# Kernel optimization log

Measured on AMD Instinct MI355X. Metric: run time of the kernel, lower is better.

Reference implementation:

```python
import jax, jax.numpy as jnp
import numpy as np

WALK_LENGTH = 8
NUM_WALKS = 5
BIRTH_DEATH_EPS = 0.1
TOLERANCE = 0.1
HALF_WIN = 16          # window is [cur-16, cur+17)
TEMP = 5.0
NEG = -1e9
EPS = 1e-8


def setup_inputs() -> dict:
    key = jax.random.key(0)
    k1, k2 = jax.random.split(key)
    seq_len, hidden = 8192, 1024
    hidden_states = jax.random.normal(k1, (seq_len, hidden), dtype=jnp.float32)
    violation_indices = jax.random.randint(k2, (1024,), 0, seq_len)
    return {"hidden_states": hidden_states, "violation_indices": violation_indices}


def _cycle_ok(row_sq, i, j, k):
    # TriadicReciprocityCheck.check_cycle, simplified algebraically:
    # M_ab = outer(b,a)/|a|^2 etc., so P = M_ca M_bc M_ab
    #      = outer(a,a) * |b|^2 |c|^2 / ((|a|^2+eps)(|b|^2+eps)(|c|^2+eps))
    # => trace(P) == fro_norm(P) == |a|^2|b|^2|c|^2 / denom  (outer(a,a) has trace=fro=|a|^2)
    na, nb, nc = row_sq[i], row_sq[j], row_sq[k]
    tr = na * nb * nc / ((na + EPS) * (nb + EPS) * (nc + EPS))
    dev = jnp.abs(tr - jnp.round(tr))
    return (dev <= TOLERANCE) & (tr <= 1.5)


def _walk(key, start, states_norm, row_sq, violation_indices):
    seq_len = states_norm.shape[0]
    offsets = jnp.arange(-HALF_WIN, HALF_WIN + 1)  # 33 local positions

    def step(carry, _):
        key, cur, prev, plen, min_sim, done, detected, aborts, restarts = carry
        key, k_samp, k_restart = jax.random.split(key, 3)
        idxs = cur + offsets
        valid = (idxs >= 0) & (idxs < seq_len)
        g = states_norm[jnp.clip(idxs, 0, seq_len - 1)]      # [33, D]
        sims = g @ states_norm[cur]                           # [33]
        logits = jnp.where(valid & (idxs != cur), sims, NEG) * TEMP
        # up to 3 multinomial attempts, each gated by the triadic reciprocity check
        samp_keys = jax.random.split(k_samp, 3)
        picks = jax.vmap(lambda k: jax.random.categorical(k, logits))(samp_keys)
        cands = cur + offsets[picks]                          # [3] candidate nodes
        ok = jax.vmap(lambda c: (plen < 2) | _cycle_ok(row_sq, prev, cur, c))(cands)
        found = jnp.any(ok)
        first = jnp.argmax(ok)
        n_aborts = jnp.where(found, first, 3).astype(jnp.int32)  # failed attempts
        cand = cands[first]
        # 'jump mental tracks': teleport to a random violation node if all attempts fail
        r = jax.random.randint(k_restart, (), 0, violation_indices.shape[0])
        restart_node = violation_indices[r]
        sim = states_norm[cur] @ states_norm[cand]
        new_min = jnp.minimum(min_sim, sim)  # path_sims min (NOT reset on restart)
        closed = found & (cand == start) & (plen > 2)
        act = ~done
        aborts = aborts + jnp.where(act, n_aborts, 0).astype(jnp.int32)
        restarts = restarts + jnp.where(act & ~found, 1, 0).astype(jnp.int32)
        detected = detected | (act & closed & (new_min < BIRTH_DEATH_EPS))
        done = done | (act & closed)
        cur2 = jnp.where(found, cand, restart_node)
        prev2 = jnp.where(found, cur, restart_node)
        plen2 = jnp.where(found, plen + 1, 1).astype(jnp.int32)
        ms2 = jnp.where(found, new_min, min_sim)
        cur = jnp.where(act, cur2, cur)
        prev = jnp.where(act, prev2, prev)
        plen = jnp.where(act, plen2, plen)
        min_sim = jnp.where(act, ms2, min_sim)
        return (key, cur, prev, plen, min_sim, done, detected, aborts, restarts), None

    init = (key, start, start, jnp.int32(1), jnp.float32(1e9),
            jnp.bool_(False), jnp.bool_(False), jnp.int32(0), jnp.int32(0))
    carry, _ = jax.lax.scan(step, init, None, length=WALK_LENGTH)
    return carry[6], carry[7], carry[8]  # detected, aborts, restarts


def reference(hidden_states, violation_indices):
    states_norm = hidden_states / (jnp.linalg.norm(hidden_states, axis=1, keepdims=True) + EPS)
    row_sq = jnp.sum(hidden_states * hidden_states, axis=1)  # |h_i|^2, for cycle check
    nv = violation_indices.shape[0]
    keys = jax.random.split(jax.random.key(42), nv * NUM_WALKS).reshape(nv, NUM_WALKS)
    walk = lambda k, s: _walk(k, s, states_norm, row_sq, violation_indices)
    det, ab, rs = jax.vmap(lambda ks, s: jax.vmap(lambda k: walk(k, s))(ks))(keys, violation_indices)
    instability_detected = jnp.any(det, axis=1)  # [num_violations] bool
    return instability_detected, jnp.sum(ab), jnp.sum(rs)
```

## Files before the change

kernel.cpp:

```cpp
#include <hip/hip_runtime.h>
#include <stdint.h>
#include <math.h>


#define HID        1024
#define NUM_WALKS  5
#define WALK_LEN   8
#define HALF_WIN   16
#define E_THRESH   1.6487212707001282

#define CENTERS    16
#define SROWS      32

__device__ __forceinline__ void tf2x32(uint32_t k0, uint32_t k1,
                                       uint32_t& x0, uint32_t& x1) {
  uint32_t ks2 = k0 ^ k1 ^ 0x1BD11BDAu;
  x0 += k0; x1 += k1;
#define TFR(r) { x0 += x1; x1 = (x1 << (r)) | (x1 >> (32 - (r))); x1 ^= x0; }
  TFR(13) TFR(15) TFR(26) TFR(6)
  x0 += k1;  x1 += ks2 + 1u;
  TFR(17) TFR(29) TFR(16) TFR(24)
  x0 += ks2; x1 += k0 + 2u;
  TFR(13) TFR(15) TFR(26) TFR(6)
  x0 += k0;  x1 += k1 + 3u;
  TFR(17) TFR(29) TFR(16) TFR(24)
  x0 += k1;  x1 += ks2 + 4u;
  TFR(13) TFR(15) TFR(26) TFR(6)
  x0 += ks2; x1 += k0 + 5u;
#undef TFR
}

__device__ __forceinline__ uint32_t tf_fold(uint32_t k0, uint32_t k1,
                                            uint32_t c0, uint32_t c1) {
  tf2x32(k0, k1, c0, c1);
  return c0 ^ c1;
}

__device__ __forceinline__ double fast_neg_log(uint32_t bits) {
  const uint32_t k = bits >> 9;
  if (k == 0) return 87.33654475055310899;
  const float u  = (float)k * 1.1920928955078125e-7f;
  const float l2 = __log2f(u);
  return (double)l2 * -0.6931471805599453;
}

__global__ __launch_bounds__(512) void band_fused_kernel(
    const float* __restrict__ H, double* __restrict__ sumsq,
    double* __restrict__ E, int* __restrict__ out, int out_n, int seq_len) {
  __shared__ __align__(16) float  tile[SROWS][HID];
  __shared__ double ssq[SROWS];

  if (blockIdx.x == 0) {
    for (int t = threadIdx.x; t < out_n; t += 512) out[t] = 0;
  }

  int wg = blockIdx.x;
  {
    const int nwg = gridDim.x;
    if ((nwg & 7) == 0) wg = (wg & 7) * (nwg >> 3) + (wg >> 3);
  }
  const int wid  = (int)(threadIdx.x >> 6);
  const int lane = (int)(threadIdx.x & 63);
  const int i0   = wg * CENTERS;
  const float4* __restrict__ H4 = (const float4*)H;

#pragma unroll
  for (int rr = 0; rr < 4; ++rr) {
    const int local = wid * 4 + rr;
    const int row   = i0 + local;
    if (row < seq_len) {
      const float4* src = H4 + ((size_t)row << 8);
      float4* dst = (float4*)&tile[local][0];
      double acc = 0.0;
#pragma unroll
      for (int k = 0; k < 4; ++k) {
        float4 x = src[lane + (k << 6)];
        dst[lane + (k << 6)] = x;
        acc += (double)x.x * x.x + (double)x.y * x.y
             + (double)x.z * x.z + (double)x.w * x.w;
      }
#pragma unroll
      for (int off = 32; off; off >>= 1) acc += __shfl_xor(acc, off);
      if (lane == 0) {
        ssq[local] = acc;
        if (local < CENTERS) sumsq[row] = acc;
      }
    }
  }
  __syncthreads();

#pragma unroll
  for (int cc = 0; cc < 2; ++cc) {
    const int cl = wid * 2 + cc;
    const int i  = i0 + cl;
    if (i >= seq_len) continue;

    float a[16];
    {
      const float4* rc = (const float4*)&tile[cl][0];
#pragma unroll
      for (int k = 0; k < 4; ++k) {
        float4 x = rc[lane + (k << 6)];
        a[4*k+0] = x.x; a[4*k+1] = x.y; a[4*k+2] = x.z; a[4*k+3] = x.w;
      }
    }
    const double ni = sqrt(ssq[cl]) + 1e-8;

    double p[16];
#pragma unroll
    for (int d = 1; d <= 16; ++d) {
      const float4* rb = (const float4*)&tile[cl + d][0];
      float ps = 0.0f;
#pragma unroll
      for (int k = 0; k < 4; ++k) {
        float4 x = rb[lane + (k << 6)];
        ps += a[4*k+0] * x.x + a[4*k+1] * x.y
            + a[4*k+2] * x.z + a[4*k+3] * x.w;
      }
      p[d-1] = (double)ps;
    }

#pragma unroll
    for (int v = 0; v < 8; ++v) {
      double send = (lane & 32) ? p[v] : p[v+8];
      double recv = __shfl_xor(send, 32);
      double mine = (lane & 32) ? p[v+8] : p[v];
      p[v] = mine + recv;
    }
#pragma unroll
    for (int v = 0; v < 4; ++v) {
      double send = (lane & 16) ? p[v] : p[v+4];
      double recv = __shfl_xor(send, 16);
      double mine = (lane & 16) ? p[v+4] : p[v];
      p[v] = mine + recv;
    }
#pragma unroll
    for (int v = 0; v < 2; ++v) {
      double send = (lane & 8) ? p[v] : p[v+2];
      double recv = __shfl_xor(send, 8);
      double mine = (lane & 8) ? p[v+2] : p[v];
      p[v] = mine + recv;
    }
    {
      double send = (lane & 4) ? p[0] : p[1];
      double recv = __shfl_xor(send, 4);
      double mine = (lane & 4) ? p[1] : p[0];
      p[0] = mine + recv;
    }
    p[0] += __shfl_xor(p[0], 2);
    p[0] += __shfl_xor(p[0], 1);

    const int v = ((lane >> 2) & 1) | (((lane >> 3) & 1) << 1)
                | (((lane >> 4) & 1) << 2) | (((lane >> 5) & 1) << 3);
    const int d = v + 1;
    if ((lane & 3) == 0 && i + d < seq_len) {
      const double s  = p[0] / (ni * (sqrt(ssq[cl + d]) + 1e-8));
      const double Ev = exp(5.0 * s);
      E[(size_t)i * 33 + 16 + d]       = Ev;
      E[(size_t)(i + d) * 33 + 16 - d] = Ev;
    }
  }
}

__global__ __launch_bounds__(256) void rowsq_kernel(
    const float* __restrict__ H, double* __restrict__ sumsq,
    int* __restrict__ out, int out_n, int seq_len) {
  if (blockIdx.x == 0) {
    for (int t = threadIdx.x; t < out_n; t += 256) out[t] = 0;
  }
  const int row  = (int)((blockIdx.x * blockDim.x + threadIdx.x) >> 6);
  const int lane = threadIdx.x & 63;
  if (row >= seq_len) return;
  const float4* r = (const float4*)(H + (size_t)row * HID);
  double acc = 0.0;
#pragma unroll
  for (int k = 0; k < 4; ++k) {
    float4 x = r[lane + (k << 6)];
    acc += (double)x.x * x.x + (double)x.y * x.y
         + (double)x.z * x.z + (double)x.w * x.w;
  }
#pragma unroll
  for (int off = 32; off; off >>= 1) acc += __shfl_xor(acc, off);
  if (lane == 0) sumsq[row] = acc;
}

__global__ __launch_bounds__(256) void walk_pre_kernel(
    const double* __restrict__ E, const double* __restrict__ sumsq,
    const int* __restrict__ viol, int* __restrict__ out,
    int nv, int seq_len) {
  int wave = (int)((blockIdx.x * blockDim.x + threadIdx.x) >> 6);
  const int lane = threadIdx.x & 63;
  if (wave >= nv * NUM_WALKS) return;
  wave = __builtin_amdgcn_readfirstlane(wave);
  const int v     = wave / NUM_WALKS;
  const int start = viol[v];

  uint32_t key0 = 0u, key1 = (uint32_t)wave;
  tf2x32(0u, 42u, key0, key1);
  key0 = __builtin_amdgcn_readfirstlane(key0);
  key1 = __builtin_amdgcn_readfirstlane(key1);

  uint32_t k0s[WALK_LEN], k1s[WALK_LEN];
#pragma unroll
  for (int s = 0; s < WALK_LEN; ++s) {
    k0s[s] = key0; k1s[s] = key1;
    uint32_t nk0 = 0u, nk1 = 0u; tf2x32(key0, key1, nk0, nk1);
    key0 = __builtin_amdgcn_readfirstlane(nk0);
    key1 = __builtin_amdgcn_readfirstlane(nk1);
  }

  const int  sl_mine = lane & 31;
  const uint32_t jpk = (uint32_t)(sl_mine + (sl_mine > 15 ? 1 : 0));
  double invwp[WALK_LEN / 2];
#pragma unroll
  for (int t = 0; t < WALK_LEN / 2; ++t) {
    uint32_t ksA0 = 0u, ksA1 = 1u; tf2x32(k0s[2*t],   k1s[2*t],   ksA0, ksA1);
    uint32_t sA0  = 0u, sA1  = 0u; tf2x32(ksA0, ksA1, sA0, sA1);
    uint32_t ksB0 = 0u, ksB1 = 1u; tf2x32(k0s[2*t+1], k1s[2*t+1], ksB0, ksB1);
    uint32_t sB0  = 0u, sB1  = 0u; tf2x32(ksB0, ksB1, sB0, sB1);
    const uint32_t s0 = (lane & 32) ? sB0 : sA0;
    const uint32_t s1 = (lane & 32) ? sB1 : sA1;
    const uint32_t bits = tf_fold(s0, s1, 0u, jpk);
    invwp[t] = 1.0 / fast_neg_log(bits);
  }

  const int sl_use = (lane < 33 && lane != HALF_WIN)
                   ? (lane - (lane > HALF_WIN)) : 0;

  int    cur = start, prev = start, plen = 1;
  double minE = 1e300;
  bool   detected = false;
  int    aborts = 0, restarts = 0;
  double na_d = sumsq[start], nb_d = na_d;

#pragma unroll
  for (int step = 0; step < WALK_LEN; ++step) {
    const int  myidx   = cur - HALF_WIN + lane;
    const bool myvalid = (lane < 33) && (lane != HALF_WIN) &&
                         (myidx >= 0) && (myidx < seq_len);
    const int  clipped = myidx < 0 ? 0 : (myidx >= seq_len ? seq_len - 1 : myidx);
    const double Ej = E[(size_t)cur * 33 + (lane < 33 ? lane : 0)];
    const double sq_win = sumsq[clipped];
    const double invw_s = __shfl(invwp[step >> 1],
                                 ((step & 1) << 5) + sl_use);

    bool found = false; int fails = 0, p = 0, cand = 0;
    double nc_d = 0.0;
    for (int at = 0; at < 3; ++at) {
      double f; int bi;
      if (myvalid) {
        if (at == 0) {
          f = Ej * invw_s;
        } else {
          uint32_t ks0 = 0u, ks1 = 1u; tf2x32(k0s[step], k1s[step], ks0, ks1);
          uint32_t s0 = 0u, s1 = (uint32_t)at; tf2x32(ks0, ks1, s0, s1);
          const uint32_t bits = tf_fold(s0, s1, 0u, (uint32_t)lane);
          f = Ej / fast_neg_log(bits);
        }
        bi = lane;
      } else { f = -1.0; bi = 1000; }
#pragma unroll
      for (int off = 32; off; off >>= 1) {
        const double of = __shfl_xor(f, off);
        const int    oi = __shfl_xor(bi, off);
        if (of > f || (of == f && oi < bi)) { f = of; bi = oi; }
      }
      p    = bi;
      cand = cur - HALF_WIN + p;
      nc_d = __shfl(sq_win, p);
      bool ok;
      if (plen < 2) ok = true;
      else {
        const float na = (float)na_d, nb = (float)nb_d, nc = (float)nc_d;
        const float tr  = (na * nb * nc) /
                          ((na + 1e-8f) * (nb + 1e-8f) * (nc + 1e-8f));
        const float dev = fabsf(tr - rintf(tr));
        ok = (dev <= 0.1f) && (tr <= 1.5f);
      }
      if (ok) { found = true; break; }
      ++fails;
    }
    aborts += fails;

    if (found) {
      const double Ewin = __shfl(Ej, p);
      minE = fmin(minE, Ewin);
      const bool closed = (cand == start) && (plen > 2);
      prev = cur; cur = cand; plen += 1;
      na_d = nb_d; nb_d = nc_d;
      if (closed) { if (minE < E_THRESH) detected = true; break; }
    } else {
      ++restarts;
      uint32_t kr0 = 0u, kr1 = 2u; tf2x32(k0s[step], k1s[step], kr0, kr1);
      uint32_t h0 = 0u, h1 = 0u; tf2x32(kr0, kr1, h0, h1);
      uint32_t l0 = 0u, l1 = 1u; tf2x32(kr0, kr1, l0, l1);
      const uint32_t hi = tf_fold(h0, h1, 0u, 0u);
      const uint32_t lo = tf_fold(l0, l1, 0u, 0u);
      const uint32_t span = (uint32_t)nv;
      uint32_t mult = (65536u % span); mult = (mult * mult) % span;
      const uint32_t r = ((hi % span) * mult + (lo % span)) % span;
      const int node = viol[r];
      cur = node; prev = node; plen = 1;
      na_d = sumsq[node]; nb_d = na_d;
    }
  }

  if (lane == 0) {
    if (detected)      atomicOr(&out[v], 1);
    if (aborts != 0)   atomicAdd(&out[nv], aborts);
    if (restarts != 0) atomicAdd(&out[nv + 1], restarts);
  }
}

__global__ __launch_bounds__(256) void walk_ref_kernel(
    const float* __restrict__ H, const int* __restrict__ viol,
    const double* __restrict__ sumsq, int* __restrict__ out,
    int nv, int seq_len) {
  const int wave = (int)((blockIdx.x * blockDim.x + threadIdx.x) >> 6);
  const int lane = threadIdx.x & 63;
  if (wave >= nv * NUM_WALKS) return;
  const int v     = wave / NUM_WALKS;
  const int start = viol[v];
  uint32_t key0 = 0u, key1 = (uint32_t)wave;
  tf2x32(0u, 42u, key0, key1);
  const float4* __restrict__ H4 = (const float4*)H;
  int    cur = start, prev = start, plen = 1;
  double min_sim = 1e9;
  bool   detected = false;
  int    aborts = 0, restarts = 0;
  for (int step = 0; step < WALK_LEN; ++step) {
    uint32_t nk0 = 0u, nk1 = 0u; tf2x32(key0, key1, nk0, nk1);
    uint32_t ks0 = 0u, ks1 = 1u; tf2x32(key0, key1, ks0, ks1);
    uint32_t kr0 = 0u, kr1 = 2u; tf2x32(key0, key1, kr0, kr1);
    const double ncur = sqrt(sumsq[cur]) + 1e-8;
    double a[16];
    {
      const float4* rc = H4 + ((size_t)cur << 8);
#pragma unroll
      for (int k = 0; k < 4; ++k) {
        float4 x = rc[lane + (k << 6)];
        a[4*k+0] = x.x; a[4*k+1] = x.y; a[4*k+2] = x.z; a[4*k+3] = x.w;
      }
    }
    double my_sim = 0.0;
    for (int jj = 0; jj < 33; ++jj) {
      const int idx = cur - HALF_WIN + jj;
      if (jj == HALF_WIN || idx < 0 || idx >= seq_len) continue;
      const float4* rb = H4 + ((size_t)idx << 8);
      double acc = 0.0;
#pragma unroll
      for (int k = 0; k < 4; ++k) {
        float4 x = rb[lane + (k << 6)];
        acc += a[4*k+0] * (double)x.x + a[4*k+1] * (double)x.y
             + a[4*k+2] * (double)x.z + a[4*k+3] * (double)x.w;
      }
#pragma unroll
      for (int off = 32; off; off >>= 1) acc += __shfl_xor(acc, off);
      const double s = acc / (ncur * (sqrt(sumsq[idx]) + 1e-8));
      if (lane == jj) my_sim = s;
    }
    bool found = false; int fails = 0, p = 0, cand = 0;
    const int  myidx   = cur - HALF_WIN + lane;
    const bool myvalid = (lane < 33) && (lane != HALF_WIN) &&
                         (myidx >= 0) && (myidx < seq_len);
    for (int at = 0; at < 3; ++at) {
      uint32_t s0 = 0u, s1 = (uint32_t)at; tf2x32(ks0, ks1, s0, s1);
      double z; int bi;
      if (myvalid) {
        const uint32_t bits = tf_fold(s0, s1, 0u, (uint32_t)lane);
        const uint32_t fb   = (bits >> 9) | 0x3f800000u;
        const float    f    = __uint_as_float(fb) - 1.0f;
        const float    u    = (f > 0.0f) ? f : 1.1754943508222875e-38f;
        const double   g    = -log(-log((double)u));
        z  = g + 5.0 * my_sim;
        bi = lane;
      } else { z = -1e300; bi = 1000; }
#pragma unroll
      for (int off = 32; off; off >>= 1) {
        const double oz = __shfl_xor(z, off);
        const int    oi = __shfl_xor(bi, off);
        if (oz > z || (oz == z && oi < bi)) { z = oz; bi = oi; }
      }
      p    = bi;
      cand = cur - HALF_WIN + p;
      bool ok;
      if (plen < 2) ok = true;
      else {
        const float na = (float)sumsq[prev], nb = (float)sumsq[cur],
                    nc = (float)sumsq[cand];
        const float tr  = (na * nb * nc) /
                          ((na + 1e-8f) * (nb + 1e-8f) * (nc + 1e-8f));
        const float dev = fabsf(tr - rintf(tr));
        ok = (dev <= 0.1f) && (tr <= 1.5f);
      }
      if (ok) { found = true; break; }
      ++fails;
    }
    aborts += fails;
    if (found) {
      const double sim = __shfl(my_sim, p);
      const double nm  = fmin(min_sim, sim);
      const bool closed = (cand == start) && (plen > 2);
      prev = cur; cur = cand; plen += 1; min_sim = nm;
      if (closed) { if (nm < 0.1) detected = true; break; }
    } else {
      ++restarts;
      uint32_t h0 = 0u, h1 = 0u; tf2x32(kr0, kr1, h0, h1);
      uint32_t l0 = 0u, l1 = 1u; tf2x32(kr0, kr1, l0, l1);
      const uint32_t hi = tf_fold(h0, h1, 0u, 0u);
      const uint32_t lo = tf_fold(l0, l1, 0u, 0u);
      const uint32_t span = (uint32_t)nv;
      uint32_t mult = (65536u % span); mult = (mult * mult) % span;
      const uint32_t r = ((hi % span) * mult + (lo % span)) % span;
      const int node = viol[r];
      cur = node; prev = node; plen = 1;
    }
    key0 = nk0; key1 = nk1;
  }
  if (lane == 0) {
    if (detected)      atomicOr(&out[v], 1);
    if (aborts != 0)   atomicAdd(&out[nv], aborts);
    if (restarts != 0) atomicAdd(&out[nv + 1], restarts);
  }
}

extern "C" void kernel_launch(void* const* d_in, const int* in_sizes, int n_in,
                              void* d_out, int out_size, void* d_ws, size_t ws_size,
                              hipStream_t stream) {
  const float* H    = (const float*)d_in[0];
  const int*   viol = (const int*)d_in[1];
  const int    nv      = in_sizes[1];
  const int    seq_len = in_sizes[0] / HID;
  const int    nwalks  = nv * NUM_WALKS;

  double* sumsq = (double*)d_ws;
  double* Etab  = (double*)((char*)d_ws + (size_t)seq_len * sizeof(double));
  const size_t need = (size_t)seq_len * sizeof(double)
                    + (size_t)seq_len * 33 * sizeof(double);

  const int wblocks = (nwalks + 3) / 4;

  if (ws_size >= need) {
    const int blocks = (seq_len + CENTERS - 1) / CENTERS;
    band_fused_kernel<<<blocks, 512, 0, stream>>>(H, sumsq, Etab,
                                                  (int*)d_out, out_size,
                                                  seq_len);
    walk_pre_kernel<<<wblocks, 256, 0, stream>>>(Etab, sumsq, viol,
                                                 (int*)d_out, nv, seq_len);
  } else {
    const int blocks = (seq_len + 3) / 4;
    rowsq_kernel<<<blocks, 256, 0, stream>>>(H, sumsq, (int*)d_out,
                                             out_size, seq_len);
    walk_ref_kernel<<<wblocks, 256, 0, stream>>>(H, viol, sumsq,
                                                 (int*)d_out, nv, seq_len);
  }
}
```

Measured before the change: 55.80 us.

## Split band tile along hidden dimension into two halves to halve LDS footprint

The shared tile shrinks from 32x1024 to 32x512 floats (128KB to 64KB), and the band dot products are computed in two passes over the hidden dimension. Partial sums are accumulated in double across the passes, and the row norms are finalised after the second pass. The smaller LDS footprint is meant to let more workgroups run per CU and overlap loads with compute, at the cost of an extra barrier pair and a second reduction sweep. Splitting the float partial sums across the passes also changes the summation order slightly.

```diff
diff --git a/kernel.cpp b/kernel.cpp
--- a/kernel.cpp
+++ b/kernel.cpp
@@ -11,6 +11,7 @@
 
 #define CENTERS    16
 #define SROWS      32
+#define KHALF      512
 
 __device__ __forceinline__ void tf2x32(uint32_t k0, uint32_t k1,
                                        uint32_t& x0, uint32_t& x1) {
@@ -47,7 +48,7 @@
 __global__ __launch_bounds__(512) void band_fused_kernel(
     const float* __restrict__ H, double* __restrict__ sumsq,
     double* __restrict__ E, int* __restrict__ out, int out_n, int seq_len) {
-  __shared__ __align__(16) float  tile[SROWS][HID];
+  __shared__ __align__(16) float  tile[SROWS][KHALF];
   __shared__ double ssq[SROWS];
 
   if (blockIdx.x == 0) {
@@ -64,97 +65,120 @@
   const int i0   = wg * CENTERS;
   const float4* __restrict__ H4 = (const float4*)H;
 
-#pragma unroll
-  for (int rr = 0; rr < 4; ++rr) {
-    const int local = wid * 4 + rr;
-    const int row   = i0 + local;
-    if (row < seq_len) {
-      const float4* src = H4 + ((size_t)row << 8);
-      float4* dst = (float4*)&tile[local][0];
-      double acc = 0.0;
-#pragma unroll
-      for (int k = 0; k < 4; ++k) {
-        float4 x = src[lane + (k << 6)];
-        dst[lane + (k << 6)] = x;
-        acc += (double)x.x * x.x + (double)x.y * x.y
-             + (double)x.z * x.z + (double)x.w * x.w;
-      }
-#pragma unroll
-      for (int off = 32; off; off >>= 1) acc += __shfl_xor(acc, off);
-      if (lane == 0) {
-        ssq[local] = acc;
-        if (local < CENTERS) sumsq[row] = acc;
-      }
-    }
-  }
-  __syncthreads();
-
+  double acc[4]  = {0.0, 0.0, 0.0, 0.0};
+  double dsum[2] = {0.0, 0.0};
+
+#pragma unroll
+  for (int half = 0; half < 2; ++half) {
+#pragma unroll
+    for (int rr = 0; rr < 4; ++rr) {
+      const int local = wid * 4 + rr;
+      const int row   = i0 + local;
+      if (row < seq_len) {
+        const float4* src = H4 + ((size_t)row << 8);
+        float4* dst = (float4*)&tile[local][0];
+#pragma unroll
+        for (int kk = 0; kk < 2; ++kk) {
+          float4 x = src[lane + ((half * 2 + kk) << 6)];
+          dst[lane + (kk << 6)] = x;
+          acc[rr] += (double)x.x * x.x + (double)x.y * x.y
+                   + (double)x.z * x.z + (double)x.w * x.w;
+        }
+      }
+    }
+    if (half == 1) {
+#pragma unroll
+      for (int rr = 0; rr < 4; ++rr) {
+        const int local = wid * 4 + rr;
+        const int row   = i0 + local;
+        if (row < seq_len) {
+          double a = acc[rr];
+#pragma unroll
+          for (int off = 32; off; off >>= 1) a += __shfl_xor(a, off);
+          if (lane == 0) {
+            ssq[local] = a;
+            if (local < CENTERS) sumsq[row] = a;
+          }
+        }
+      }
+    }
+    __syncthreads();
+
+#pragma unroll
+    for (int cc = 0; cc < 2; ++cc) {
+      const int cl = wid * 2 + cc;
+      const int i  = i0 + cl;
+      if (i >= seq_len) continue;
+
+      float a[8];
+      {
+        const float4* rc = (const float4*)&tile[cl][0];
+#pragma unroll
+        for (int kk = 0; kk < 2; ++kk) {
+          float4 x = rc[lane + (kk << 6)];
+          a[4*kk+0] = x.x; a[4*kk+1] = x.y; a[4*kk+2] = x.z; a[4*kk+3] = x.w;
+        }
+      }
+
+      double p[16];
+#pragma unroll
+      for (int d = 1; d <= 16; ++d) {
+        const float4* rb = (const float4*)&tile[cl + d][0];
+        float ps = 0.0f;
+#pragma unroll
+        for (int kk = 0; kk < 2; ++kk) {
+          float4 x = rb[lane + (kk << 6)];
+          ps += a[4*kk+0] * x.x + a[4*kk+1] * x.y
+              + a[4*kk+2] * x.z + a[4*kk+3] * x.w;
+        }
+        p[d-1] = (double)ps;
+      }
+
+#pragma unroll
+      for (int v = 0; v < 8; ++v) {
+        double send = (lane & 32) ? p[v] : p[v+8];
+        double recv = __shfl_xor(send, 32);
+        double mine = (lane & 32) ? p[v+8] : p[v];
+        p[v] = mine + recv;
+      }
+#pragma unroll
+      for (int v = 0; v < 4; ++v) {
+        double send = (lane & 16) ? p[v] : p[v+4];
+        double recv = __shfl_xor(send, 16);
+        double mine = (lane & 16) ? p[v+4] : p[v];
+        p[v] = mine + recv;
+      }
+#pragma unroll
+      for (int v = 0; v < 2; ++v) {
+        double send = (lane & 8) ? p[v] : p[v+2];
+        double recv = __shfl_xor(send, 8);
+        double mine = (lane & 8) ? p[v+2] : p[v];
+        p[v] = mine + recv;
+      }
+      {
+        double send = (lane & 4) ? p[0] : p[1];
+        double recv = __shfl_xor(send, 4);
+        double mine = (lane & 4) ? p[1] : p[0];
+        p[0] = mine + recv;
+      }
+      p[0] += __shfl_xor(p[0], 2);
+      p[0] += __shfl_xor(p[0], 1);
+
+      dsum[cc] += p[0];
+    }
+    __syncthreads();
+  }
+
+  const int v = ((lane >> 2) & 1) | (((lane >> 3) & 1) << 1)
+              | (((lane >> 4) & 1) << 2) | (((lane >> 5) & 1) << 3);
+  const int d = v + 1;
 #pragma unroll
   for (int cc = 0; cc < 2; ++cc) {
     const int cl = wid * 2 + cc;
     const int i  = i0 + cl;
-    if (i >= seq_len) continue;
-
-    float a[16];
-    {
-      const float4* rc = (const float4*)&tile[cl][0];
-#pragma unroll
-      for (int k = 0; k < 4; ++k) {
-        float4 x = rc[lane + (k << 6)];
-        a[4*k+0] = x.x; a[4*k+1] = x.y; a[4*k+2] = x.z; a[4*k+3] = x.w;
-      }
-    }
-    const double ni = sqrt(ssq[cl]) + 1e-8;
-
-    double p[16];
-#pragma unroll
-    for (int d = 1; d <= 16; ++d) {
-      const float4* rb = (const float4*)&tile[cl + d][0];
-      float ps = 0.0f;
-#pragma unroll
-      for (int k = 0; k < 4; ++k) {
-        float4 x = rb[lane + (k << 6)];
-        ps += a[4*k+0] * x.x + a[4*k+1] * x.y
-            + a[4*k+2] * x.z + a[4*k+3] * x.w;
-      }
-      p[d-1] = (double)ps;
-    }
-
-#pragma unroll
-    for (int v = 0; v < 8; ++v) {
-      double send = (lane & 32) ? p[v] : p[v+8];
-      double recv = __shfl_xor(send, 32);
-      double mine = (lane & 32) ? p[v+8] : p[v];
-      p[v] = mine + recv;
-    }
-#pragma unroll
-    for (int v = 0; v < 4; ++v) {
-      double send = (lane & 16) ? p[v] : p[v+4];
-      double recv = __shfl_xor(send, 16);
-      double mine = (lane & 16) ? p[v+4] : p[v];
-      p[v] = mine + recv;
-    }
-#pragma unroll
-    for (int v = 0; v < 2; ++v) {
-      double send = (lane & 8) ? p[v] : p[v+2];
-      double recv = __shfl_xor(send, 8);
-      double mine = (lane & 8) ? p[v+2] : p[v];
-      p[v] = mine + recv;
-    }
-    {
-      double send = (lane & 4) ? p[0] : p[1];
-      double recv = __shfl_xor(send, 4);
-      double mine = (lane & 4) ? p[1] : p[0];
-      p[0] = mine + recv;
-    }
-    p[0] += __shfl_xor(p[0], 2);
-    p[0] += __shfl_xor(p[0], 1);
-
-    const int v = ((lane >> 2) & 1) | (((lane >> 3) & 1) << 1)
-                | (((lane >> 4) & 1) << 2) | (((lane >> 5) & 1) << 3);
-    const int d = v + 1;
-    if ((lane & 3) == 0 && i + d < seq_len) {
-      const double s  = p[0] / (ni * (sqrt(ssq[cl + d]) + 1e-8));
+    if (i < seq_len && (lane & 3) == 0 && i + d < seq_len) {
+      const double ni = sqrt(ssq[cl]) + 1e-8;
+      const double s  = dsum[cc] / (ni * (sqrt(ssq[cl + d]) + 1e-8));
       const double Ev = exp(5.0 * s);
       E[(size_t)i * 33 + 16 + d]       = Ev;
       E[(size_t)(i + d) * 33 + 16 - d] = Ev;
```

After: 54.14 us. -3.0%, faster.
